# Kernel tuning notes

Measured on AMD Instinct MI355X. Metric: run time of the kernel, lower is better.

## Reference

```python
import jax, jax.numpy as jnp
import numpy as np

N_NODES = 100000
N_EDGES = 320000
HID = 256
NE = 128  # node_embed_dim = hid // 2 (use_stats=True, sgrl=False)
N_LAYERS = 3

NET, DEV, PIN = 0, 1, 2


def setup_inputs() -> dict:
    key = jax.random.key(0)
    ks = jax.random.split(key, 24)
    s = 0.05
    inp = {
        "node_attr": jax.random.uniform(ks[0], (N_NODES, 17), dtype=jnp.float32),
        "y": jax.random.uniform(ks[1], (N_NODES, 2), dtype=jnp.float32),
        "node_emb": jax.random.normal(ks[2], (4, NE), dtype=jnp.float32) * s,
        "edge_emb": jax.random.normal(ks[3], (4, HID), dtype=jnp.float32) * s,
        "net_W": jax.random.normal(ks[4], (17, NE), dtype=jnp.float32) * s,
        "net_b": jnp.zeros((NE,), jnp.float32),
        "dev_W": jax.random.normal(ks[5], (17, NE), dtype=jnp.float32) * s,
        "dev_b": jnp.zeros((NE,), jnp.float32),
        "pin_emb": jax.random.normal(ks[6], (17, NE), dtype=jnp.float32) * s,
        "sage_Wl": jax.random.normal(ks[7], (N_LAYERS, HID, HID), dtype=jnp.float32) * s,
        "sage_bl": jnp.zeros((N_LAYERS, HID), jnp.float32),
        "sage_Wr": jax.random.normal(ks[8], (N_LAYERS, HID, HID), dtype=jnp.float32) * s,
        "head_W0": jax.random.normal(ks[9], (HID, HID), dtype=jnp.float32) * s,
        "head_b0": jnp.zeros((HID,), jnp.float32),
        "head_W1": jax.random.normal(ks[10], (HID, 1), dtype=jnp.float32) * s,
        "head_b1": jnp.zeros((1,), jnp.float32),
        "node_type": jax.random.randint(ks[11], (N_NODES,), 0, 4, dtype=jnp.int32),
        "edge_type": jax.random.randint(ks[12], (N_EDGES,), 0, 4, dtype=jnp.int32),
        "edge_index": jax.random.randint(ks[13], (2, N_EDGES), 0, N_NODES, dtype=jnp.int32),
    }
    return inp


def _forward(node_attr, y, node_emb, edge_emb, net_W, net_b, dev_W, dev_b,
             pin_emb, sage_Wl, sage_bl, sage_Wr, head_W0, head_b0, head_W1,
             head_b1, node_type, edge_type, edge_index):
    # node / edge type encoders (embedding lookups)
    x = node_emb[node_type]                 # [N, NE]
    xe = edge_emb[edge_type]                # [N_E, HID] (unused by SAGE, kept for fidelity)
    del xe

    # per-type attribute embedding, scattered into a zero tensor via disjoint masks
    net_mask = node_type == NET
    dev_mask = node_type == DEV
    pin_mask = node_type == PIN
    net_e = node_attr @ net_W + net_b       # [N, NE]
    dev_e = node_attr @ dev_W + dev_b       # [N, NE]
    pin_idx = node_attr[:, 0].astype(jnp.int32)
    pin_e = pin_emb[pin_idx]                # [N, NE]
    attr_emb = jnp.where(net_mask[:, None], net_e,
                jnp.where(dev_mask[:, None], dev_e,
                jnp.where(pin_mask[:, None], pin_e, jnp.zeros_like(net_e))))
    x = jnp.concatenate([x, attr_emb], axis=1)  # [N, HID]

    src, dst = edge_index[0], edge_index[1]
    cnt = jax.ops.segment_sum(jnp.ones_like(src, dtype=x.dtype), dst,
                              num_segments=N_NODES)
    denom = jnp.maximum(cnt, 1.0)[:, None]
    for l in range(N_LAYERS):
        # SAGEConv: mean-aggregate neighbor features, then two linear maps
        agg = jax.ops.segment_sum(x[src], dst, num_segments=N_NODES) / denom
        x = agg @ sage_Wl[l] + sage_bl[l] + x @ sage_Wr[l]
        x = jax.nn.relu(x)

    # head MLP (2 layers): Linear -> ReLU -> Linear
    h = jax.nn.relu(x @ head_W0 + head_b0)
    pred = h @ head_W1 + head_b1            # [N, 1]
    true_class = y[:, 1].astype(jnp.int32)
    true_label = y
    return pred, true_class, true_label


def reference(node_attr, y, node_emb, edge_emb, net_W, net_b, dev_W, dev_b,
              pin_emb, sage_Wl, sage_bl, sage_Wr, head_W0, head_b0, head_W1,
              head_b1, node_type, edge_type, edge_index):
    return _forward(node_attr, y, node_emb, edge_emb, net_W, net_b, dev_W,
                    dev_b, pin_emb, sage_Wl, sage_bl, sage_Wr, head_W0,
                    head_b0, head_W1, head_b1, node_type, edge_type,
                    edge_index)
```

## Files before the change

### kernel.cpp

```cpp
#include <hip/hip_runtime.h>
#include <hip/hip_bf16.h>

#define N_NODES 100000
#define N_EDGES 320000
#define HID 256
#define NE 128
#define NLAYERS 3

typedef __attribute__((ext_vector_type(8))) short short8;
typedef __attribute__((ext_vector_type(4))) float f32x4;

__device__ inline float bfbits2f(unsigned int b) { return __uint_as_float(b << 16); }

__device__ inline unsigned int pack_bf2(float lo, float hi) {
    __hip_bfloat16 l = __float2bfloat16(lo), h = __float2bfloat16(hi);
    return (unsigned int)*(unsigned short*)&l |
           ((unsigned int)*(unsigned short*)&h << 16);
}

__global__ __launch_bounds__(256) void k_prep(
    const float* __restrict__ Wl, const float* __restrict__ Wr,
    const float* __restrict__ W0,
    __hip_bfloat16* __restrict__ Wt, __hip_bfloat16* __restrict__ Wh,
    int* __restrict__ deg, int* __restrict__ total)
{
    int t = blockIdx.x * 256 + threadIdx.x;
    const int total_sage = 3 * 256 * 512;
    if (t < total_sage) {
        int l = t >> 17;
        int rem = t & 131071;
        int n = rem >> 9;
        int k = rem & 511;
        const float* Wsrc = (k < 256) ? (Wl + (size_t)l * 65536)
                                      : (Wr + (size_t)l * 65536);
        Wt[t] = __float2bfloat16(Wsrc[(k & 255) * 256 + n]);
    } else {
        int u = t - total_sage;
        if (u < 65536) {
            int n = u >> 8, k = u & 255;
            Wh[u] = __float2bfloat16(W0[k * 256 + n]);
        }
    }
    if (t < N_NODES) deg[t] = 0;
    if (t == 0) *total = 0;
}

__global__ __launch_bounds__(256) void k_init(
    const float* __restrict__ node_attr,
    const float* __restrict__ node_emb,
    const float* __restrict__ net_W, const float* __restrict__ net_b,
    const float* __restrict__ dev_W, const float* __restrict__ dev_b,
    const float* __restrict__ pin_emb,
    const int*   __restrict__ node_type,
    const float* __restrict__ y, const float* __restrict__ b1,
    float* __restrict__ out,
    __hip_bfloat16* __restrict__ x)
{
    int t = blockIdx.x * 256 + threadIdx.x;
    if (t < N_NODES * 32) {
        int n  = t >> 5;
        int c4 = (t & 31) * 4;
        int ty = node_type[n];
        float4 e = *(const float4*)(node_emb + ty * NE + c4);
        float4 a;
        if (ty == 0 || ty == 1) {
            const float* W = (ty == 0) ? net_W : dev_W;
            const float* b = (ty == 0) ? net_b : dev_b;
            a = *(const float4*)(b + c4);
            const float* ar = node_attr + (size_t)n * 17;
            #pragma unroll
            for (int k = 0; k < 17; ++k) {
                float av = ar[k];
                float4 wv = *(const float4*)(W + k * NE + c4);
                a.x += av * wv.x; a.y += av * wv.y;
                a.z += av * wv.z; a.w += av * wv.w;
            }
        } else if (ty == 2) {
            int idx = (int)node_attr[(size_t)n * 17];
            a = *(const float4*)(pin_emb + idx * NE + c4);
        } else {
            a.x = a.y = a.z = a.w = 0.0f;
        }
        uint2 ev = {pack_bf2(e.x, e.y), pack_bf2(e.z, e.w)};
        uint2 av = {pack_bf2(a.x, a.y), pack_bf2(a.z, a.w)};
        *(uint2*)((char*)x + (size_t)n * 512 + c4 * 2)       = ev;
        *(uint2*)((char*)x + (size_t)n * 512 + 256 + c4 * 2) = av;
    } else {
        int n = t - N_NODES * 32;
        if (n < N_NODES) {
            float y0 = y[(size_t)n * 2 + 0];
            float y1 = y[(size_t)n * 2 + 1];
            out[n] = b1[0];
            out[N_NODES + n] = (float)(int)y1;
            out[2 * N_NODES + 2 * n + 0] = y0;
            out[2 * N_NODES + 2 * n + 1] = y1;
        }
    }
}

__global__ __launch_bounds__(256) void k_hist(
    const int* __restrict__ edge_index, int* __restrict__ deg)
{
    int e = blockIdx.x * 256 + threadIdx.x;
    if (e < N_EDGES) atomicAdd(&deg[edge_index[N_EDGES + e]], 1);
}

__global__ __launch_bounds__(256) void k_alloc(
    const int* __restrict__ deg, int* __restrict__ off,
    int* __restrict__ cursor, int* __restrict__ total)
{
    int n = blockIdx.x * 256 + threadIdx.x;
    int lane = threadIdx.x & 63;
    int d = (n < N_NODES) ? deg[n] : 0;
    int incl = d;
    #pragma unroll
    for (int o = 1; o < 64; o <<= 1) {
        int v = __shfl_up(incl, o, 64);
        if (lane >= o) incl += v;
    }
    int wtot = __shfl(incl, 63, 64);
    int base = 0;
    if (lane == 63) base = atomicAdd(total, wtot);
    base = __shfl(base, 63, 64);
    if (n < N_NODES) {
        int o = base + incl - d;
        off[n] = o;
        cursor[n] = o;
    }
}

__global__ __launch_bounds__(256) void k_fill(
    const int* __restrict__ edge_index, int* __restrict__ cursor,
    int* __restrict__ slots)
{
    int e = blockIdx.x * 256 + threadIdx.x;
    if (e >= N_EDGES) return;
    int s = edge_index[e];
    int d = edge_index[N_EDGES + e];
    int slot = atomicAdd(&cursor[d], 1);
    slots[slot] = s;
}

__global__ __launch_bounds__(256) void k_aggregate(
    const __hip_bfloat16* __restrict__ x,
    const int* __restrict__ off, const int* __restrict__ deg,
    const int* __restrict__ slots,
    __hip_bfloat16* __restrict__ agg)
{
    int g = blockIdx.x * 256 + threadIdx.x;
    int wid = g >> 6;
    int lane = g & 63;
    int sub = lane >> 4;
    int l16 = lane & 15;
    int n = wid * 4 + sub;
    bool active = n < N_NODES;
    int o = 0, d = 0;
    if (active) { o = off[n]; d = deg[n]; }
    float acc[16];
    #pragma unroll
    for (int i = 0; i < 16; ++i) acc[i] = 0.0f;
    for (int p = 0; p < d; ++p) {
        int src = slots[o + p];
        const char* rp = (const char*)x + (size_t)src * 512 + l16 * 32;
        uint4 v0 = *(const uint4*)rp;
        uint4 v1 = *(const uint4*)(rp + 16);
        const unsigned int u[8] = {v0.x, v0.y, v0.z, v0.w, v1.x, v1.y, v1.z, v1.w};
        #pragma unroll
        for (int i = 0; i < 8; ++i) {
            acc[2 * i + 0] += bfbits2f(u[i] & 0xffffu);
            acc[2 * i + 1] += __uint_as_float(u[i] & 0xffff0000u);
        }
    }
    if (active) {
        float rs = 1.0f / fmaxf((float)d, 1.0f);
        unsigned int w[8];
        #pragma unroll
        for (int i = 0; i < 8; ++i)
            w[i] = pack_bf2(acc[2 * i + 0] * rs, acc[2 * i + 1] * rs);
        uint4 o0 = {w[0], w[1], w[2], w[3]};
        uint4 o1 = {w[4], w[5], w[6], w[7]};
        char* op = (char*)agg + (size_t)n * 512 + l16 * 32;
        *(uint4*)op = o0;
        *(uint4*)(op + 16) = o1;
    }
}

template <bool SAGE>
__global__ __launch_bounds__(512, 4) void k_mfma(
    const __hip_bfloat16* __restrict__ Agg,
    const __hip_bfloat16* __restrict__ X,
    const __hip_bfloat16* __restrict__ Wt,
    const float* __restrict__ bias,
    const float* __restrict__ W1,
    __hip_bfloat16* __restrict__ Out,
    float* __restrict__ Pred)
{
    __shared__ char As[2][16384];

    const int tid  = threadIdx.x;
    const int w    = tid >> 6, lane = tid & 63;
    const int l15  = lane & 15, lg = lane >> 4;
    const int row0 = blockIdx.x * 128;
    const int KT     = SAGE ? 512 : 256;
    const int nsteps = SAGE ? 8 : 4;

    f32x4 acc[8][2];
    #pragma unroll
    for (int i = 0; i < 8; ++i)
        #pragma unroll
        for (int n = 0; n < 2; ++n) acc[i][n] = (f32x4)0.0f;

    const int srow   = tid >> 3;
    const int schunk = tid & 7;

    auto stage = [&](int s, int b) {
        const char* base;
        int k0;
        if (SAGE && s < 4) { base = (const char*)Agg; k0 = s * 64; }
        else               { base = (const char*)X;   k0 = (SAGE ? s - 4 : s) * 64; }
        #pragma unroll
        for (int issue = 0; issue < 2; ++issue) {
            int row  = srow + issue * 64;
            int grow = row0 + row;
            if (grow >= N_NODES) grow = N_NODES - 1;
            const char* gp = base + (size_t)grow * 512 + (size_t)k0 * 2
                           + ((schunk ^ (row & 7)) << 4);
            const char* lp = &As[b][issue * 8192 + tid * 16];
            __builtin_amdgcn_global_load_lds(
                (const __attribute__((address_space(1))) void*)gp,
                (__attribute__((address_space(3))) void*)lp, 16, 0, 0);
        }
    };

    auto loadB = [&](int s, short8 (&bb)[2][2]) {
        #pragma unroll
        for (int h = 0; h < 2; ++h)
            #pragma unroll
            for (int n = 0; n < 2; ++n) {
                int c = w * 32 + n * 16 + l15;
                bb[h][n] = *(const short8*)(Wt + (size_t)c * KT + s * 64 + h * 32 + 8 * lg);
            }
    };

    auto do_step = [&](int s, bool last, short8 (&bcur)[2][2], short8 (&bnxt)[2][2]) {
        const int b = s & 1;
        if (last) asm volatile("s_waitcnt vmcnt(0)" ::: "memory");
        else      asm volatile("s_waitcnt vmcnt(2)" ::: "memory");
        __builtin_amdgcn_sched_barrier(0);
        __builtin_amdgcn_s_barrier();
        __builtin_amdgcn_sched_barrier(0);
        if (!last) loadB(s + 1, bnxt);
        #pragma unroll
        for (int h = 0; h < 2; ++h) {
            #pragma unroll
            for (int i = 0; i < 8; ++i) {
                int r = i * 16 + l15;
                short8 a = *(const short8*)&As[b][r * 128 + (((lg + 4 * h) ^ (r & 7)) << 4)];
                acc[i][0] = __builtin_amdgcn_mfma_f32_16x16x32_bf16(a, bcur[h][0], acc[i][0], 0, 0, 0);
                acc[i][1] = __builtin_amdgcn_mfma_f32_16x16x32_bf16(a, bcur[h][1], acc[i][1], 0, 0, 0);
            }
        }
        __builtin_amdgcn_sched_barrier(0);
        __builtin_amdgcn_s_barrier();
        __builtin_amdgcn_sched_barrier(0);
        if (s + 2 < nsteps) stage(s + 2, b);
    };

    short8 b0[2][2], b1[2][2];
    loadB(0, b0);
    stage(0, 0);
    stage(1, 1);
    #pragma unroll
    for (int s = 0; s < nsteps; s += 2) {
        do_step(s,     s == nsteps - 1, b0, b1);
        do_step(s + 1, s + 1 == nsteps - 1, b1, b0);
    }

    if (SAGE) {
        __hip_bfloat16* lo = (__hip_bfloat16*)As;
        #pragma unroll
        for (int hh = 0; hh < 2; ++hh) {
            #pragma unroll
            for (int n = 0; n < 2; ++n) {
                int c = w * 32 + n * 16 + l15;
                float bv = bias[c];
                #pragma unroll
                for (int i2 = 0; i2 < 4; ++i2) {
                    int i = hh * 4 + i2;
                    #pragma unroll
                    for (int r = 0; r < 4; ++r) {
                        int rl = i2 * 16 + lg * 4 + r;
                        lo[rl * 256 + c] = __float2bfloat16(fmaxf(acc[i][n][r] + bv, 0.0f));
                    }
                }
            }
            __syncthreads();
            #pragma unroll
            for (int q = 0; q < 4; ++q) {
                int chunk = tid + q * 512;
                int rl = chunk >> 5, cc = chunk & 31;
                int grow = row0 + hh * 64 + rl;
                if (grow < N_NODES)
                    *(uint4*)((char*)Out + (size_t)grow * 512 + cc * 16) =
                        *(const uint4*)((const char*)As + rl * 512 + cc * 16);
            }
            __syncthreads();
        }
    } else {
        #pragma unroll
        for (int i = 0; i < 8; ++i) {
            float p[4];
            #pragma unroll
            for (int r = 0; r < 4; ++r) p[r] = 0.0f;
            #pragma unroll
            for (int n = 0; n < 2; ++n) {
                int c = w * 32 + n * 16 + l15;
                float bv = bias[c];
                float wv = W1[c];
                #pragma unroll
                for (int r = 0; r < 4; ++r)
                    p[r] += fmaxf(acc[i][n][r] + bv, 0.0f) * wv;
            }
            #pragma unroll
            for (int r = 0; r < 4; ++r) {
                float s = p[r];
                #pragma unroll
                for (int m = 1; m < 16; m <<= 1) s += __shfl_xor(s, m, 64);
                if (l15 == 0) {
                    int row = row0 + i * 16 + lg * 4 + r;
                    if (row < N_NODES) atomicAdd(&Pred[row], s);
                }
            }
        }
    }
}

extern "C" void kernel_launch(void* const* d_in, const int* in_sizes, int n_in,
                              void* d_out, int out_size, void* d_ws, size_t ws_size,
                              hipStream_t stream) {
    const float* node_attr = (const float*)d_in[0];
    const float* y         = (const float*)d_in[1];
    const float* node_emb  = (const float*)d_in[2];
    const float* net_W     = (const float*)d_in[4];
    const float* net_b     = (const float*)d_in[5];
    const float* dev_W     = (const float*)d_in[6];
    const float* dev_b     = (const float*)d_in[7];
    const float* pin_emb   = (const float*)d_in[8];
    const float* sage_Wl   = (const float*)d_in[9];
    const float* sage_bl   = (const float*)d_in[10];
    const float* sage_Wr   = (const float*)d_in[11];
    const float* head_W0   = (const float*)d_in[12];
    const float* head_b0   = (const float*)d_in[13];
    const float* head_W1   = (const float*)d_in[14];
    const float* head_b1   = (const float*)d_in[15];
    const int*   node_type = (const int*)d_in[16];
    const int*   edge_idx  = (const int*)d_in[18];
    float* out = (float*)d_out;

    const size_t xelems = (size_t)N_NODES * HID;
    char* p = (char*)d_ws;
    __hip_bfloat16* x0  = (__hip_bfloat16*)p;  p += xelems * 2;
    __hip_bfloat16* x1  = (__hip_bfloat16*)p;  p += xelems * 2;
    __hip_bfloat16* agg = (__hip_bfloat16*)p;  p += xelems * 2;
    __hip_bfloat16* Wt  = (__hip_bfloat16*)p;  p += (size_t)3 * 256 * 512 * 2;
    __hip_bfloat16* Wh  = (__hip_bfloat16*)p;  p += (size_t)256 * 256 * 2;
    int* deg    = (int*)p; p += N_NODES * 4;
    int* off    = (int*)p; p += N_NODES * 4;
    int* cursor = (int*)p; p += N_NODES * 4;
    int* slots  = (int*)p; p += N_EDGES * 4;
    int* total  = (int*)p; p += 16;

    k_prep<<<(3 * 131072 + 65536 + 255) / 256, 256, 0, stream>>>(
        sage_Wl, sage_Wr, head_W0, Wt, Wh, deg, total);
    k_init<<<(N_NODES * 33 + 255) / 256, 256, 0, stream>>>(
        node_attr, node_emb, net_W, net_b, dev_W, dev_b, pin_emb, node_type,
        y, head_b1, out, x0);
    k_hist<<<(N_EDGES + 255) / 256, 256, 0, stream>>>(edge_idx, deg);
    k_alloc<<<(N_NODES + 255) / 256, 256, 0, stream>>>(deg, off, cursor, total);
    k_fill<<<(N_EDGES + 255) / 256, 256, 0, stream>>>(edge_idx, cursor, slots);

    const int gemm_grid = (N_NODES + 127) / 128;
    __hip_bfloat16* xcur = x0;
    __hip_bfloat16* xalt = x1;
    for (int l = 0; l < NLAYERS; ++l) {
        k_aggregate<<<(N_NODES / 4 * 64 + 255) / 256, 256, 0, stream>>>(
            xcur, off, deg, slots, agg);
        k_mfma<true><<<gemm_grid, 512, 0, stream>>>(
            agg, xcur, Wt + (size_t)l * 131072,
            sage_bl + (size_t)l * HID, nullptr, xalt, nullptr);
        __hip_bfloat16* t = xcur; xcur = xalt; xalt = t;
    }
    k_mfma<false><<<gemm_grid, 512, 0, stream>>>(
        xcur, xcur, Wh, head_b0, head_W1, nullptr, out);
}
```

Measured before the change: 360.1 us.

## Fuse neighbor mean-aggregation into the SAGE GEMM producer stage

Removes the separate aggregation kernel and its intermediate agg buffer. The SAGE GEMM kernel now gathers and averages neighbor rows itself for the first four K-steps, writing them into swizzled LDS while MFMAs run on the previous buffer. The head GEMM is split out as its own kernel. This saves the agg write and reread and one launch per layer, but the register-held gather loop of variable degree now sits inside the GEMM pipeline, which can stall the MFMA schedule and lowers occupancy (launch bounds 512,3).

```diff
diff --git a/kernel.cpp b/kernel.cpp
--- a/kernel.cpp
+++ b/kernel.cpp
@@ -141,59 +141,13 @@
     slots[slot] = s;
 }
 
-__global__ __launch_bounds__(256) void k_aggregate(
-    const __hip_bfloat16* __restrict__ x,
+__global__ __launch_bounds__(512, 3) void k_sage(
+    const __hip_bfloat16* __restrict__ X,
     const int* __restrict__ off, const int* __restrict__ deg,
     const int* __restrict__ slots,
-    __hip_bfloat16* __restrict__ agg)
-{
-    int g = blockIdx.x * 256 + threadIdx.x;
-    int wid = g >> 6;
-    int lane = g & 63;
-    int sub = lane >> 4;
-    int l16 = lane & 15;
-    int n = wid * 4 + sub;
-    bool active = n < N_NODES;
-    int o = 0, d = 0;
-    if (active) { o = off[n]; d = deg[n]; }
-    float acc[16];
-    #pragma unroll
-    for (int i = 0; i < 16; ++i) acc[i] = 0.0f;
-    for (int p = 0; p < d; ++p) {
-        int src = slots[o + p];
-        const char* rp = (const char*)x + (size_t)src * 512 + l16 * 32;
-        uint4 v0 = *(const uint4*)rp;
-        uint4 v1 = *(const uint4*)(rp + 16);
-        const unsigned int u[8] = {v0.x, v0.y, v0.z, v0.w, v1.x, v1.y, v1.z, v1.w};
-        #pragma unroll
-        for (int i = 0; i < 8; ++i) {
-            acc[2 * i + 0] += bfbits2f(u[i] & 0xffffu);
-            acc[2 * i + 1] += __uint_as_float(u[i] & 0xffff0000u);
-        }
-    }
-    if (active) {
-        float rs = 1.0f / fmaxf((float)d, 1.0f);
-        unsigned int w[8];
-        #pragma unroll
-        for (int i = 0; i < 8; ++i)
-            w[i] = pack_bf2(acc[2 * i + 0] * rs, acc[2 * i + 1] * rs);
-        uint4 o0 = {w[0], w[1], w[2], w[3]};
-        uint4 o1 = {w[4], w[5], w[6], w[7]};
-        char* op = (char*)agg + (size_t)n * 512 + l16 * 32;
-        *(uint4*)op = o0;
-        *(uint4*)(op + 16) = o1;
-    }
-}
-
-template <bool SAGE>
-__global__ __launch_bounds__(512, 4) void k_mfma(
-    const __hip_bfloat16* __restrict__ Agg,
-    const __hip_bfloat16* __restrict__ X,
     const __hip_bfloat16* __restrict__ Wt,
     const float* __restrict__ bias,
-    const float* __restrict__ W1,
-    __hip_bfloat16* __restrict__ Out,
-    float* __restrict__ Pred)
+    __hip_bfloat16* __restrict__ Out)
 {
     __shared__ char As[2][16384];
 
@@ -201,8 +155,6 @@
     const int w    = tid >> 6, lane = tid & 63;
     const int l15  = lane & 15, lg = lane >> 4;
     const int row0 = blockIdx.x * 128;
-    const int KT     = SAGE ? 512 : 256;
-    const int nsteps = SAGE ? 8 : 4;
 
     f32x4 acc[8][2];
     #pragma unroll
@@ -210,20 +162,52 @@
         #pragma unroll
         for (int n = 0; n < 2; ++n) acc[i][n] = (f32x4)0.0f;
 
+    const int gr = tid >> 2;
+    const int gq = tid & 2 ? (tid & 3) : (tid & 3);
+    const int grow = row0 + gr;
+    int go = 0, gd = 0;
+    if (grow < N_NODES) { go = off[grow]; gd = deg[grow]; }
+    const float grs = 1.0f / fmaxf((float)gd, 1.0f);
+
     const int srow   = tid >> 3;
     const int schunk = tid & 7;
 
-    auto stage = [&](int s, int b) {
-        const char* base;
-        int k0;
-        if (SAGE && s < 4) { base = (const char*)Agg; k0 = s * 64; }
-        else               { base = (const char*)X;   k0 = (SAGE ? s - 4 : s) * 64; }
+    auto produce_gather = [&](int s, int b) {
+        float a[16];
+        #pragma unroll
+        for (int i = 0; i < 16; ++i) a[i] = 0.0f;
+        for (int p = 0; p < gd; ++p) {
+            int src = slots[go + p];
+            const char* rp = (const char*)X + (size_t)src * 512 + s * 128 + gq * 32;
+            uint4 v0 = *(const uint4*)rp;
+            uint4 v1 = *(const uint4*)(rp + 16);
+            unsigned int u[8] = {v0.x, v0.y, v0.z, v0.w, v1.x, v1.y, v1.z, v1.w};
+            #pragma unroll
+            for (int i = 0; i < 8; ++i) {
+                a[2 * i + 0] += bfbits2f(u[i] & 0xffffu);
+                a[2 * i + 1] += __uint_as_float(u[i] & 0xffff0000u);
+            }
+        }
+        unsigned int wo[8];
+        #pragma unroll
+        for (int i = 0; i < 8; ++i)
+            wo[i] = pack_bf2(a[2 * i + 0] * grs, a[2 * i + 1] * grs);
+        uint4 w0 = {wo[0], wo[1], wo[2], wo[3]};
+        uint4 w1 = {wo[4], wo[5], wo[6], wo[7]};
+        int c0 = gq * 2;
+        char* bp = &As[b][0];
+        *(uint4*)(bp + gr * 128 + (((c0    ) ^ (gr & 7)) << 4)) = w0;
+        *(uint4*)(bp + gr * 128 + (((c0 + 1) ^ (gr & 7)) << 4)) = w1;
+    };
+
+    auto produce_x = [&](int s, int b) {
+        int k0b = (s - 4) * 128;
         #pragma unroll
         for (int issue = 0; issue < 2; ++issue) {
             int row  = srow + issue * 64;
-            int grow = row0 + row;
-            if (grow >= N_NODES) grow = N_NODES - 1;
-            const char* gp = base + (size_t)grow * 512 + (size_t)k0 * 2
+            int grw  = row0 + row;
+            if (grw >= N_NODES) grw = N_NODES - 1;
+            const char* gp = (const char*)X + (size_t)grw * 512 + k0b
                            + ((schunk ^ (row & 7)) << 4);
             const char* lp = &As[b][issue * 8192 + tid * 16];
             __builtin_amdgcn_global_load_lds(
@@ -238,18 +222,17 @@
             #pragma unroll
             for (int n = 0; n < 2; ++n) {
                 int c = w * 32 + n * 16 + l15;
-                bb[h][n] = *(const short8*)(Wt + (size_t)c * KT + s * 64 + h * 32 + 8 * lg);
-            }
-    };
-
-    auto do_step = [&](int s, bool last, short8 (&bcur)[2][2], short8 (&bnxt)[2][2]) {
+                bb[h][n] = *(const short8*)(Wt + (size_t)c * 512 + s * 64 + h * 32 + 8 * lg);
+            }
+    };
+
+    auto do_step = [&](int s, short8 (&bcur)[2][2], short8 (&bnxt)[2][2]) {
         const int b = s & 1;
-        if (last) asm volatile("s_waitcnt vmcnt(0)" ::: "memory");
-        else      asm volatile("s_waitcnt vmcnt(2)" ::: "memory");
-        __builtin_amdgcn_sched_barrier(0);
-        __builtin_amdgcn_s_barrier();
-        __builtin_amdgcn_sched_barrier(0);
-        if (!last) loadB(s + 1, bnxt);
+        if (s + 1 < 8) {
+            if (s + 1 < 4) produce_gather(s + 1, b ^ 1);
+            else           produce_x(s + 1, b ^ 1);
+            loadB(s + 1, bnxt);
+        }
         #pragma unroll
         for (int h = 0; h < 2; ++h) {
             #pragma unroll
@@ -260,23 +243,30 @@
                 acc[i][1] = __builtin_amdgcn_mfma_f32_16x16x32_bf16(a, bcur[h][1], acc[i][1], 0, 0, 0);
             }
         }
+        asm volatile("s_waitcnt vmcnt(4) lgkmcnt(0)" ::: "memory");
         __builtin_amdgcn_sched_barrier(0);
         __builtin_amdgcn_s_barrier();
         __builtin_amdgcn_sched_barrier(0);
-        if (s + 2 < nsteps) stage(s + 2, b);
     };
 
     short8 b0[2][2], b1[2][2];
+    produce_gather(0, 0);
     loadB(0, b0);
-    stage(0, 0);
-    stage(1, 1);
-    #pragma unroll
-    for (int s = 0; s < nsteps; s += 2) {
-        do_step(s,     s == nsteps - 1, b0, b1);
-        do_step(s + 1, s + 1 == nsteps - 1, b1, b0);
-    }
-
-    if (SAGE) {
+    asm volatile("s_waitcnt lgkmcnt(0)" ::: "memory");
+    __builtin_amdgcn_sched_barrier(0);
+    __builtin_amdgcn_s_barrier();
+    __builtin_amdgcn_sched_barrier(0);
+
+    do_step(0, b0, b1);
+    do_step(1, b1, b0);
+    do_step(2, b0, b1);
+    do_step(3, b1, b0);
+    do_step(4, b0, b1);
+    do_step(5, b1, b0);
+    do_step(6, b0, b1);
+    do_step(7, b1, b0);
+
+    {
         __hip_bfloat16* lo = (__hip_bfloat16*)As;
         #pragma unroll
         for (int hh = 0; hh < 2; ++hh) {
@@ -299,37 +289,121 @@
             for (int q = 0; q < 4; ++q) {
                 int chunk = tid + q * 512;
                 int rl = chunk >> 5, cc = chunk & 31;
-                int grow = row0 + hh * 64 + rl;
-                if (grow < N_NODES)
-                    *(uint4*)((char*)Out + (size_t)grow * 512 + cc * 16) =
+                int grw = row0 + hh * 64 + rl;
+                if (grw < N_NODES)
+                    *(uint4*)((char*)Out + (size_t)grw * 512 + cc * 16) =
                         *(const uint4*)((const char*)As + rl * 512 + cc * 16);
             }
             __syncthreads();
         }
-    } else {
-        #pragma unroll
-        for (int i = 0; i < 8; ++i) {
-            float p[4];
-            #pragma unroll
-            for (int r = 0; r < 4; ++r) p[r] = 0.0f;
+    }
+}
+
+__global__ __launch_bounds__(512, 4) void k_head(
+    const __hip_bfloat16* __restrict__ X,
+    const __hip_bfloat16* __restrict__ Wt,
+    const float* __restrict__ bias,
+    const float* __restrict__ W1,
+    float* __restrict__ Pred)
+{
+    __shared__ char As[2][16384];
+
+    const int tid  = threadIdx.x;
+    const int w    = tid >> 6, lane = tid & 63;
+    const int l15  = lane & 15, lg = lane >> 4;
+    const int row0 = blockIdx.x * 128;
+    const int nsteps = 4;
+
+    f32x4 acc[8][2];
+    #pragma unroll
+    for (int i = 0; i < 8; ++i)
+        #pragma unroll
+        for (int n = 0; n < 2; ++n) acc[i][n] = (f32x4)0.0f;
+
+    const int srow   = tid >> 3;
+    const int schunk = tid & 7;
+
+    auto stage = [&](int s, int b) {
+        int k0b = s * 128;
+        #pragma unroll
+        for (int issue = 0; issue < 2; ++issue) {
+            int row  = srow + issue * 64;
+            int grow = row0 + row;
+            if (grow >= N_NODES) grow = N_NODES - 1;
+            const char* gp = (const char*)X + (size_t)grow * 512 + k0b
+                           + ((schunk ^ (row & 7)) << 4);
+            const char* lp = &As[b][issue * 8192 + tid * 16];
+            __builtin_amdgcn_global_load_lds(
+                (const __attribute__((address_space(1))) void*)gp,
+                (__attribute__((address_space(3))) void*)lp, 16, 0, 0);
+        }
+    };
+
+    auto loadB = [&](int s, short8 (&bb)[2][2]) {
+        #pragma unroll
+        for (int h = 0; h < 2; ++h)
             #pragma unroll
             for (int n = 0; n < 2; ++n) {
                 int c = w * 32 + n * 16 + l15;
-                float bv = bias[c];
-                float wv = W1[c];
-                #pragma unroll
-                for (int r = 0; r < 4; ++r)
-                    p[r] += fmaxf(acc[i][n][r] + bv, 0.0f) * wv;
-            }
-            #pragma unroll
-            for (int r = 0; r < 4; ++r) {
-                float s = p[r];
-                #pragma unroll
-                for (int m = 1; m < 16; m <<= 1) s += __shfl_xor(s, m, 64);
-                if (l15 == 0) {
-                    int row = row0 + i * 16 + lg * 4 + r;
-                    if (row < N_NODES) atomicAdd(&Pred[row], s);
-                }
+                bb[h][n] = *(const short8*)(Wt + (size_t)c * 256 + s * 64 + h * 32 + 8 * lg);
+            }
+    };
+
+    auto do_step = [&](int s, bool last, short8 (&bcur)[2][2], short8 (&bnxt)[2][2]) {
+        const int b = s & 1;
+        if (last) asm volatile("s_waitcnt vmcnt(0)" ::: "memory");
+        else      asm volatile("s_waitcnt vmcnt(2)" ::: "memory");
+        __builtin_amdgcn_sched_barrier(0);
+        __builtin_amdgcn_s_barrier();
+        __builtin_amdgcn_sched_barrier(0);
+        if (!last) loadB(s + 1, bnxt);
+        #pragma unroll
+        for (int h = 0; h < 2; ++h) {
+            #pragma unroll
+            for (int i = 0; i < 8; ++i) {
+                int r = i * 16 + l15;
+                short8 a = *(const short8*)&As[b][r * 128 + (((lg + 4 * h) ^ (r & 7)) << 4)];
+                acc[i][0] = __builtin_amdgcn_mfma_f32_16x16x32_bf16(a, bcur[h][0], acc[i][0], 0, 0, 0);
+                acc[i][1] = __builtin_amdgcn_mfma_f32_16x16x32_bf16(a, bcur[h][1], acc[i][1], 0, 0, 0);
+            }
+        }
+        __builtin_amdgcn_sched_barrier(0);
+        __builtin_amdgcn_s_barrier();
+        __builtin_amdgcn_sched_barrier(0);
+        if (s + 2 < nsteps) stage(s + 2, b);
+    };
+
+    short8 b0[2][2], b1[2][2];
+    loadB(0, b0);
+    stage(0, 0);
+    stage(1, 1);
+    do_step(0, false, b0, b1);
+    do_step(1, false, b1, b0);
+    do_step(2, false, b0, b1);
+    do_step(3, true,  b1, b0);
+
+    #pragma unroll
+    for (int i = 0; i < 8; ++i) {
+        float p[4];
+        #pragma unroll
+        for (int r = 0; r < 4; ++r) p[r] = 0.0f;
+        #pragma unroll
+        for (int n = 0; n < 2; ++n) {
+            int c = w * 32 + n * 16 + l15;
+            float bv = bias[c];
+            float wv = W1[c];
+            #pragma unroll
+            for (int r = 0; r < 4; ++r)
+                p[r] += fmaxf(acc[i][n][r] + bv, 0.0f) * wv;
+        }
+        #pragma unroll
+        for (int r = 0; r < 4; ++r) {
+            float s = p[r];
+            #pragma unroll
+            for (int m = 1; m < 16; m <<= 1) s += __shfl_xor(s, m, 64);
+            if (l15 == 0) {
+                int row = row0 + i * 16 + lg * 4 + r;
+                if (row < N_NODES) atomicAdd(&Pred[row], s);
             }
         }
     }
@@ -361,7 +435,6 @@
     char* p = (char*)d_ws;
     __hip_bfloat16* x0  = (__hip_bfloat16*)p;  p += xelems * 2;
     __hip_bfloat16* x1  = (__hip_bfloat16*)p;  p += xelems * 2;
-    __hip_bfloat16* agg = (__hip_bfloat16*)p;  p += xelems * 2;
     __hip_bfloat16* Wt  = (__hip_bfloat16*)p;  p += (size_t)3 * 256 * 512 * 2;
     __hip_bfloat16* Wh  = (__hip_bfloat16*)p;  p += (size_t)256 * 256 * 2;
     int* deg    = (int*)p; p += N_NODES * 4;
@@ -383,13 +456,11 @@
     __hip_bfloat16* xcur = x0;
     __hip_bfloat16* xalt = x1;
     for (int l = 0; l < NLAYERS; ++l) {
-        k_aggregate<<<(N_NODES / 4 * 64 + 255) / 256, 256, 0, stream>>>(
-            xcur, off, deg, slots, agg);
-        k_mfma<true><<<gemm_grid, 512, 0, stream>>>(
-            agg, xcur, Wt + (size_t)l * 131072,
-            sage_bl + (size_t)l * HID, nullptr, xalt, nullptr);
+        k_sage<<<gemm_grid, 512, 0, stream>>>(
+            xcur, off, deg, slots, Wt + (size_t)l * 131072,
+            sage_bl + (size_t)l * HID, xalt);
         __hip_bfloat16* t = xcur; xcur = xalt; xalt = t;
     }
-    k_mfma<false><<<gemm_grid, 512, 0, stream>>>(
-        xcur, xcur, Wh, head_b0, head_W1, nullptr, out);
-}
+    k_head<<<gemm_grid, 512, 0, stream>>>(
+        xcur, Wh, head_b0, head_W1, out);
+}
```

After: 506.9 us. 1.41x slower.

## Triple-buffer MFMA LDS staging with one barrier per step; fuse degree histogram into init

Applied to the files above, without the earlier changes.

The GEMM kernel's LDS A-tile staging moves from double to triple buffering. This removes the second barrier per k-step and issues the next-next stage load before the MFMA loop, so global loads overlap compute with less synchronisation. The k-loop is fully unrolled by hand and launch bounds ask for 6 blocks per CU, but 48KB of LDS per block may limit occupancy. The separate degree-histogram kernel is folded into the init kernel as extra threads, saving one launch.

```diff
diff --git a/kernel.cpp b/kernel.cpp
--- a/kernel.cpp
+++ b/kernel.cpp
@@ -53,6 +53,7 @@
     const float* __restrict__ pin_emb,
     const int*   __restrict__ node_type,
     const float* __restrict__ y, const float* __restrict__ b1,
+    const int*   __restrict__ edge_index, int* __restrict__ deg,
     float* __restrict__ out,
     __hip_bfloat16* __restrict__ x)
 {
@@ -85,24 +86,18 @@
         uint2 av = {pack_bf2(a.x, a.y), pack_bf2(a.z, a.w)};
         *(uint2*)((char*)x + (size_t)n * 512 + c4 * 2)       = ev;
         *(uint2*)((char*)x + (size_t)n * 512 + 256 + c4 * 2) = av;
+    } else if (t < N_NODES * 33) {
+        int n = t - N_NODES * 32;
+        float y0 = y[(size_t)n * 2 + 0];
+        float y1 = y[(size_t)n * 2 + 1];
+        out[n] = b1[0];
+        out[N_NODES + n] = (float)(int)y1;
+        out[2 * N_NODES + 2 * n + 0] = y0;
+        out[2 * N_NODES + 2 * n + 1] = y1;
     } else {
-        int n = t - N_NODES * 32;
-        if (n < N_NODES) {
-            float y0 = y[(size_t)n * 2 + 0];
-            float y1 = y[(size_t)n * 2 + 1];
-            out[n] = b1[0];
-            out[N_NODES + n] = (float)(int)y1;
-            out[2 * N_NODES + 2 * n + 0] = y0;
-            out[2 * N_NODES + 2 * n + 1] = y1;
-        }
-    }
-}
-
-__global__ __launch_bounds__(256) void k_hist(
-    const int* __restrict__ edge_index, int* __restrict__ deg)
-{
-    int e = blockIdx.x * 256 + threadIdx.x;
-    if (e < N_EDGES) atomicAdd(&deg[edge_index[N_EDGES + e]], 1);
+        int e = t - N_NODES * 33;
+        if (e < N_EDGES) atomicAdd(&deg[edge_index[N_EDGES + e]], 1);
+    }
 }
 
 __global__ __launch_bounds__(256) void k_alloc(
@@ -186,7 +181,7 @@
 }
 
 template <bool SAGE>
-__global__ __launch_bounds__(512, 4) void k_mfma(
+__global__ __launch_bounds__(512, 6) void k_mfma(
     const __hip_bfloat16* __restrict__ Agg,
     const __hip_bfloat16* __restrict__ X,
     const __hip_bfloat16* __restrict__ Wt,
@@ -195,7 +190,7 @@
     __hip_bfloat16* __restrict__ Out,
     float* __restrict__ Pred)
 {
-    __shared__ char As[2][16384];
+    __shared__ char As[3][16384];
 
     const int tid  = threadIdx.x;
     const int w    = tid >> 6, lane = tid & 63;
@@ -213,7 +208,8 @@
     const int srow   = tid >> 3;
     const int schunk = tid & 7;
 
-    auto stage = [&](int s, int b) {
+    auto stage = [&](int s) {
+        const int b = s % 3;
         const char* base;
         int k0;
         if (SAGE && s < 4) { base = (const char*)Agg; k0 = s * 64; }
@@ -243,13 +239,14 @@
     };
 
     auto do_step = [&](int s, bool last, short8 (&bcur)[2][2], short8 (&bnxt)[2][2]) {
-        const int b = s & 1;
+        const int b = s % 3;
         if (last) asm volatile("s_waitcnt vmcnt(0)" ::: "memory");
         else      asm volatile("s_waitcnt vmcnt(2)" ::: "memory");
         __builtin_amdgcn_sched_barrier(0);
         __builtin_amdgcn_s_barrier();
         __builtin_amdgcn_sched_barrier(0);
         if (!last) loadB(s + 1, bnxt);
+        if (s + 2 < nsteps) stage(s + 2);
         #pragma unroll
         for (int h = 0; h < 2; ++h) {
             #pragma unroll
@@ -260,23 +257,30 @@
                 acc[i][1] = __builtin_amdgcn_mfma_f32_16x16x32_bf16(a, bcur[h][1], acc[i][1], 0, 0, 0);
             }
         }
-        __builtin_amdgcn_sched_barrier(0);
-        __builtin_amdgcn_s_barrier();
-        __builtin_amdgcn_sched_barrier(0);
-        if (s + 2 < nsteps) stage(s + 2, b);
     };
 
     short8 b0[2][2], b1[2][2];
     loadB(0, b0);
-    stage(0, 0);
-    stage(1, 1);
-    #pragma unroll
-    for (int s = 0; s < nsteps; s += 2) {
-        do_step(s,     s == nsteps - 1, b0, b1);
-        do_step(s + 1, s + 1 == nsteps - 1, b1, b0);
-    }
-
+    stage(0);
+    stage(1);
     if (SAGE) {
+        do_step(0, false, b0, b1);
+        do_step(1, false, b1, b0);
+        do_step(2, false, b0, b1);
+        do_step(3, false, b1, b0);
+        do_step(4, false, b0, b1);
+        do_step(5, false, b1, b0);
+        do_step(6, false, b0, b1);
+        do_step(7, true,  b1, b0);
+    } else {
+        do_step(0, false, b0, b1);
+        do_step(1, false, b1, b0);
+        do_step(2, false, b0, b1);
+        do_step(3, true,  b1, b0);
+    }
+
+    if (SAGE) {
+        __syncthreads();
         __hip_bfloat16* lo = (__hip_bfloat16*)As;
         #pragma unroll
         for (int hh = 0; hh < 2; ++hh) {
@@ -372,10 +376,9 @@
 
     k_prep<<<(3 * 131072 + 65536 + 255) / 256, 256, 0, stream>>>(
         sage_Wl, sage_Wr, head_W0, Wt, Wh, deg, total);
-    k_init<<<(N_NODES * 33 + 255) / 256, 256, 0, stream>>>(
+    k_init<<<(N_NODES * 33 + N_EDGES + 255) / 256, 256, 0, stream>>>(
         node_attr, node_emb, net_W, net_b, dev_W, dev_b, pin_emb, node_type,
-        y, head_b1, out, x0);
-    k_hist<<<(N_EDGES + 255) / 256, 256, 0, stream>>>(edge_idx, deg);
+        y, head_b1, edge_idx, deg, out, x0);
     k_alloc<<<(N_NODES + 255) / 256, 256, 0, stream>>>(deg, off, cursor, total);
     k_fill<<<(N_EDGES + 255) / 256, 256, 0, stream>>>(edge_idx, cursor, slots);
 
```

After: 715.6 us. +98.7%, slower.
